# Kernel optimization log

Measured on AMD Instinct MI355X. Metric: run time of the kernel, lower is better.

The kernel has to match this reference:

```python
import jax, jax.numpy as jnp
import numpy as np

BETA = 0.25

def setup_inputs() -> dict:
    key = jax.random.key(0)
    k1, k2 = jax.random.split(key)
    N, D, K = 262144, 64, 512
    encoding = jax.random.normal(k1, (N, D), dtype=jnp.float32)
    # original inits uniform(-1/K, 1/K); scale a normal similarly is fine, but stay faithful:
    weight = jax.random.uniform(k2, (K, D), dtype=jnp.float32, minval=-1.0 / K, maxval=1.0 / K)
    return {"encoding": encoding, "weight": weight}


def reference(encoding, weight):
    # flat view: encoding already [N, D]
    x = encoding  # [N, D]
    # squared euclidean distances; argmin is invariant to sqrt and to ||x||^2 term
    x2 = jnp.sum(x * x, axis=1, keepdims=True)            # [N, 1]
    w2 = jnp.sum(weight * weight, axis=1)                  # [K]
    d2 = x2 - 2.0 * (x @ weight.T) + w2[None, :]           # [N, K]
    idx = jnp.argmin(d2, axis=1)                           # [N]
    quantized = weight[idx]                                # gather == one_hot @ weight, [N, D]

    commitment_loss = jnp.mean((jax.lax.stop_gradient(quantized) - x) ** 2)
    embedding_loss = jnp.mean((quantized - jax.lax.stop_gradient(x)) ** 2)
    vq_loss = commitment_loss * BETA + embedding_loss

    # straight-through estimator
    quantized_st = x + jax.lax.stop_gradient(quantized - x)
    return (idx[:, None], quantized_st, vq_loss)
```

## Files before the change

### kernel.cpp

```cpp
#include <hip/hip_runtime.h>

#define NROWS 262144
#define DDIM  64
#define KCB   512

#define MARGKEY (3u << 17)

#define WS_CNT   0
#define WS_W2P3  1024
#define WS_WHI   4096
#define WS_WMID  69632
#define WS_LIST  135168

typedef __attribute__((ext_vector_type(8))) short short8;
typedef __attribute__((ext_vector_type(4))) float floatx4;

__device__ __forceinline__ unsigned umin2(unsigned a, unsigned b) { return a < b ? a : b; }
__device__ __forceinline__ unsigned umax2(unsigned a, unsigned b) { return a > b ? a : b; }

__device__ __forceinline__ float np_sumsq64(const float* a) {
    float r[8];
#pragma unroll
    for (int j = 0; j < 8; ++j) r[j] = __fmul_rn(a[j], a[j]);
#pragma unroll
    for (int i = 8; i < 64; i += 8) {
#pragma unroll
        for (int j = 0; j < 8; ++j)
            r[j] = __fadd_rn(r[j], __fmul_rn(a[i + j], a[i + j]));
    }
    return __fadd_rn(__fadd_rn(__fadd_rn(r[0], r[1]), __fadd_rn(r[2], r[3])),
                     __fadd_rn(__fadd_rn(r[4], r[5]), __fadd_rn(r[6], r[7])));
}

__device__ __forceinline__ void split2(float e0, float e1, unsigned& hid, unsigned& mid) {
    unsigned u0 = __float_as_uint(e0), u1 = __float_as_uint(e1);
    float r0 = __fsub_rn(e0, __uint_as_float(u0 & 0xFFFF0000u));
    float r1 = __fsub_rn(e1, __uint_as_float(u1 & 0xFFFF0000u));
    hid = (u0 >> 16) | (u1 & 0xFFFF0000u);
    mid = (__float_as_uint(r0) >> 16) | (__float_as_uint(r1) & 0xFFFF0000u);
}

__global__ void vq_prep(const float* __restrict__ w, float* __restrict__ w2p3,
                        unsigned short* __restrict__ whi,
                        unsigned short* __restrict__ wmid) {
    const int k = threadIdx.x;
    float ws[64];
    const float4* wp = (const float4*)(w + (size_t)k * DDIM);
#pragma unroll
    for (int j = 0; j < 16; ++j) {
        float4 v = wp[j];
        ws[4 * j + 0] = v.x; ws[4 * j + 1] = v.y;
        ws[4 * j + 2] = v.z; ws[4 * j + 3] = v.w;
    }
    w2p3[k] = __fadd_rn(np_sumsq64(ws), 3.0f);
#pragma unroll
    for (int d = 0; d < 64; ++d) {
        float v = __fmul_rn(-2.0f, ws[d]);
        unsigned u = __float_as_uint(v);
        whi[k * 64 + d] = (unsigned short)(u >> 16);
        float rem = __fsub_rn(v, __uint_as_float(u & 0xFFFF0000u));
        wmid[k * 64 + d] = (unsigned short)(__float_as_uint(rem) >> 16);
    }
}

__launch_bounds__(512, 4)
__global__ void vq_gemm(const float* __restrict__ x,
                        const unsigned short* __restrict__ whi,
                        const unsigned short* __restrict__ wmid,
                        const float* __restrict__ w2p3g,
                        float* __restrict__ out_idx,
                        unsigned* __restrict__ cnt,
                        unsigned* __restrict__ list, int listcap) {
    const int tid = threadIdx.x;
    const int wave = tid >> 6, lane = tid & 63;
    const int n16 = lane & 15, quad = lane >> 4;

    __shared__ float w2p3s[KCB];
    __shared__ __align__(16) unsigned sbh[2][16 * 36];
    __shared__ __align__(16) unsigned sbm[2][16 * 36];
    __shared__ uint2 mm[8][32][16];

    w2p3s[tid] = w2p3g[tid];

    short8 ah[4][2], am[4][2];
#pragma unroll
    for (int f = 0; f < 4; ++f) {
        const int cw = wave * 64 + f * 16 + n16;
#pragma unroll
        for (int s = 0; s < 2; ++s) {
            ah[f][s] = *(const short8*)(whi + (size_t)cw * 64 + s * 32 + quad * 8);
            am[f][s] = *(const short8*)(wmid + (size_t)cw * 64 + s * 32 + quad * 8);
        }
    }

    const int r0 = blockIdx.x * 512;
    const int srow = tid >> 5, sj2 = tid & 31;
    {
        float2 v = *(const float2*)(x + (size_t)(r0 + srow) * DDIM + 2 * sj2);
        unsigned hid, mid; split2(v.x, v.y, hid, mid);
        sbh[0][srow * 36 + sj2] = hid;
        sbm[0][srow * 36 + sj2] = mid;
    }
    __syncthreads();

    const unsigned cwq = (unsigned)(wave * 64 + quad * 4);

    for (int it = 0; it < 32; ++it) {
        const int p = it & 1;
        float2 pre;
        if (it < 31)
            pre = *(const float2*)(x + (size_t)(r0 + (it + 1) * 16 + srow) * DDIM + 2 * sj2);

        short8 b_h0 = *(const short8*)&sbh[p][n16 * 36 + quad * 4];
        short8 b_h1 = *(const short8*)&sbh[p][n16 * 36 + 16 + quad * 4];
        short8 b_m0 = *(const short8*)&sbm[p][n16 * 36 + quad * 4];
        short8 b_m1 = *(const short8*)&sbm[p][n16 * 36 + 16 + quad * 4];

        floatx4 acc[4];
#pragma unroll
        for (int f = 0; f < 4; ++f)
            acc[f] = *(const floatx4*)&w2p3s[wave * 64 + f * 16 + quad * 4];
#pragma unroll
        for (int f = 0; f < 4; ++f) {
            acc[f] = __builtin_amdgcn_mfma_f32_16x16x32_bf16(ah[f][0], b_h0, acc[f], 0, 0, 0);
            acc[f] = __builtin_amdgcn_mfma_f32_16x16x32_bf16(ah[f][0], b_m0, acc[f], 0, 0, 0);
            acc[f] = __builtin_amdgcn_mfma_f32_16x16x32_bf16(am[f][0], b_h0, acc[f], 0, 0, 0);
            acc[f] = __builtin_amdgcn_mfma_f32_16x16x32_bf16(ah[f][1], b_h1, acc[f], 0, 0, 0);
            acc[f] = __builtin_amdgcn_mfma_f32_16x16x32_bf16(ah[f][1], b_m1, acc[f], 0, 0, 0);
            acc[f] = __builtin_amdgcn_mfma_f32_16x16x32_bf16(am[f][1], b_h1, acc[f], 0, 0, 0);
        }

        unsigned m1 = 0xFFFFFFFFu, m2 = 0xFFFFFFFFu;
#pragma unroll
        for (int f = 0; f < 4; ++f) {
#pragma unroll
            for (int reg = 0; reg < 4; ++reg) {
                unsigned key = (__float_as_uint(acc[f][reg]) << 9) +
                               (cwq + (unsigned)(f * 16 + reg));
                unsigned t = umax2(m1, key);
                m2 = umin2(m2, t);
                m1 = umin2(m1, key);
            }
        }
#pragma unroll
        for (int s = 16; s <= 32; s <<= 1) {
            unsigned o1 = __shfl_xor((int)m1, s);
            unsigned o2 = __shfl_xor((int)m2, s);
            m2 = umin2(umin2(m2, o2), umax2(m1, o1));
            m1 = umin2(m1, o1);
        }
        if (lane < 16) mm[wave][it][n16] = make_uint2(m1, m2);

        if (it < 31) {
            unsigned hid, mid; split2(pre.x, pre.y, hid, mid);
            sbh[p ^ 1][srow * 36 + sj2] = hid;
            sbm[p ^ 1][srow * 36 + sj2] = mid;
        }
        __syncthreads();
    }

    unsigned a1 = 0xFFFFFFFFu, a2 = 0xFFFFFFFFu;
#pragma unroll
    for (int wv = 0; wv < 8; ++wv) {
        uint2 v = mm[wv][tid >> 4][tid & 15];
        a2 = umin2(umin2(a2, v.y), umax2(a1, v.x));
        a1 = umin2(a1, v.x);
    }
    out_idx[r0 + tid] = (float)(a1 & 511u);
    bool flag = (a2 - a1 < MARGKEY);
    unsigned long long mask = __ballot(flag);
    int nw = __popcll(mask);
    unsigned base = 0;
    if (lane == 0 && nw) base = atomicAdd(cnt, (unsigned)nw);
    base = (unsigned)__shfl((int)base, 0);
    if (flag) {
        unsigned pos = base + (unsigned)__popcll(mask & ((1ull << lane) - 1ull));
        if ((int)pos < listcap) list[pos] = (unsigned)(r0 + tid);
    }
}

__launch_bounds__(512, 4)
__global__ void vq_recheck(const float* __restrict__ x,
                           const float* __restrict__ w,
                           const unsigned* __restrict__ cnt,
                           const unsigned* __restrict__ list, int listcap,
                           float* __restrict__ out_idx) {
    const int tid = threadIdx.x;
    unsigned total = *cnt;
    if (total > (unsigned)listcap) total = (unsigned)listcap;
    const unsigned nb = (total + 15) >> 4;

    float wl[64];
    {
        const float4* wp = (const float4*)(w + (size_t)tid * DDIM);
#pragma unroll
        for (int j = 0; j < 16; ++j) {
            float4 v = wp[j];
            wl[4 * j + 0] = v.x; wl[4 * j + 1] = v.y;
            wl[4 * j + 2] = v.z; wl[4 * j + 3] = v.w;
        }
    }
    const float w2l = np_sumsq64(wl);

    __shared__ float d2tile[16][KCB];
    __shared__ int rowbuf[16];
    __shared__ float x2buf[16];

    for (unsigned batch = blockIdx.x; batch < nb; batch += gridDim.x) {
        if (tid < 16) {
            unsigned li = batch * 16 + (unsigned)tid;
            rowbuf[tid] = (li < total) ? (int)list[li] : -1;
        }
        __syncthreads();

        if (tid < 128) {
            const int rl = tid >> 3, j = tid & 7;
            int row = rowbuf[rl]; if (row < 0) row = 0;
            const float* xr = x + (size_t)row * DDIM;
            float a0 = xr[j];
            float r = __fmul_rn(a0, a0);
#pragma unroll
            for (int i = 1; i < 8; ++i) {
                float ai = xr[8 * i + j];
                r = __fadd_rn(r, __fmul_rn(ai, ai));
            }
            float s1 = __fadd_rn(r,  __shfl_xor(r, 1));
            float s2 = __fadd_rn(s1, __shfl_xor(s1, 2));
            float s4 = __fadd_rn(s2, __shfl_xor(s2, 4));
            if (j == 0) x2buf[rl] = s4;
        }
        __syncthreads();

        for (int g = 0; g < 16; g += 4) {
            int ra = rowbuf[g + 0]; if (ra < 0) ra = 0;
            int rb = rowbuf[g + 1]; if (rb < 0) rb = 0;
            int rc = rowbuf[g + 2]; if (rc < 0) rc = 0;
            int rd = rowbuf[g + 3]; if (rd < 0) rd = 0;
            const float* xr0 = x + (size_t)ra * DDIM;
            const float* xr1 = x + (size_t)rb * DDIM;
            const float* xr2 = x + (size_t)rc * DDIM;
            const float* xr3 = x + (size_t)rd * DDIM;
            float m0 = 0.f, m1 = 0.f, m2 = 0.f, m3 = 0.f;
#pragma unroll
            for (int jb = 0; jb < 16; ++jb) {
                float4 a0 = *(const float4*)(xr0 + 4 * jb);
                float4 a1 = *(const float4*)(xr1 + 4 * jb);
                float4 a2 = *(const float4*)(xr2 + 4 * jb);
                float4 a3 = *(const float4*)(xr3 + 4 * jb);
                m0 = __fmaf_rn(a0.x, wl[4 * jb + 0], m0);
                m0 = __fmaf_rn(a0.y, wl[4 * jb + 1], m0);
                m0 = __fmaf_rn(a0.z, wl[4 * jb + 2], m0);
                m0 = __fmaf_rn(a0.w, wl[4 * jb + 3], m0);
                m1 = __fmaf_rn(a1.x, wl[4 * jb + 0], m1);
                m1 = __fmaf_rn(a1.y, wl[4 * jb + 1], m1);
                m1 = __fmaf_rn(a1.z, wl[4 * jb + 2], m1);
                m1 = __fmaf_rn(a1.w, wl[4 * jb + 3], m1);
                m2 = __fmaf_rn(a2.x, wl[4 * jb + 0], m2);
                m2 = __fmaf_rn(a2.y, wl[4 * jb + 1], m2);
                m2 = __fmaf_rn(a2.z, wl[4 * jb + 2], m2);
                m2 = __fmaf_rn(a2.w, wl[4 * jb + 3], m2);
                m3 = __fmaf_rn(a3.x, wl[4 * jb + 0], m3);
                m3 = __fmaf_rn(a3.y, wl[4 * jb + 1], m3);
                m3 = __fmaf_rn(a3.z, wl[4 * jb + 2], m3);
                m3 = __fmaf_rn(a3.w, wl[4 * jb + 3], m3);
            }
            float X0 = x2buf[g + 0], X1 = x2buf[g + 1];
            float X2 = x2buf[g + 2], X3 = x2buf[g + 3];
            d2tile[g + 0][tid] = __fadd_rn(__fsub_rn(X0, __fmul_rn(2.0f, m0)), w2l);
            d2tile[g + 1][tid] = __fadd_rn(__fsub_rn(X1, __fmul_rn(2.0f, m1)), w2l);
            d2tile[g + 2][tid] = __fadd_rn(__fsub_rn(X2, __fmul_rn(2.0f, m2)), w2l);
            d2tile[g + 3][tid] = __fadd_rn(__fsub_rn(X3, __fmul_rn(2.0f, m3)), w2l);
        }
        __syncthreads();

        {
            const int rl  = tid >> 5;
            const int sub = tid & 31;
            float bv = d2tile[rl][sub];
            int   bi = sub;
#pragma unroll
            for (int i = 1; i < 16; ++i) {
                int cc = sub + 32 * i;
                float v = d2tile[rl][cc];
                if (v < bv) { bv = v; bi = cc; }
            }
#pragma unroll
            for (int s = 1; s < 32; s <<= 1) {
                float ov = __shfl_xor(bv, s);
                int   oi = __shfl_xor(bi, s);
                if (ov < bv || (ov == bv && oi < bi)) { bv = ov; bi = oi; }
            }
            if (sub == 0 && rowbuf[rl] >= 0) out_idx[rowbuf[rl]] = (float)bi;
        }
        __syncthreads();
    }
}

__launch_bounds__(256)
__global__ void vq_epilogue(const float* __restrict__ x,
                            const float* __restrict__ w,
                            const float* __restrict__ out_idx_f,
                            float* __restrict__ out_q,
                            float* __restrict__ out_loss) {
    const int row  = blockIdx.x * blockDim.x + threadIdx.x;
    const int bidx = (int)out_idx_f[row];

    const float4* xp = (const float4*)(x + (size_t)row * DDIM);
    const float4* wq = (const float4*)(w + (size_t)bidx * DDIM);
    float4* qo = (float4*)(out_q + (size_t)row * DDIM);
    float ls = 0.0f;
#pragma unroll
    for (int j = 0; j < 16; ++j) {
        float4 xv = xp[j];
        float4 wv = wq[j];
        float e0 = __fsub_rn(wv.x, xv.x), e1 = __fsub_rn(wv.y, xv.y);
        float e2 = __fsub_rn(wv.z, xv.z), e3 = __fsub_rn(wv.w, xv.w);
        ls = fmaf(e0, e0, ls); ls = fmaf(e1, e1, ls);
        ls = fmaf(e2, e2, ls); ls = fmaf(e3, e3, ls);
        float4 q;
        q.x = __fadd_rn(xv.x, e0); q.y = __fadd_rn(xv.y, e1);
        q.z = __fadd_rn(xv.z, e2); q.w = __fadd_rn(xv.w, e3);
        qo[j] = q;
    }
#pragma unroll
    for (int off = 32; off > 0; off >>= 1) ls += __shfl_down(ls, off);
    __shared__ float red[4];
    const int lane = threadIdx.x & 63;
    const int wid  = threadIdx.x >> 6;
    if (lane == 0) red[wid] = ls;
    __syncthreads();
    if (threadIdx.x == 0) {
        float t = (red[0] + red[1]) + (red[2] + red[3]);
        atomicAdd(out_loss, t * (1.25f / (float)(NROWS * DDIM)));
    }
}

extern "C" void kernel_launch(void* const* d_in, const int* in_sizes, int n_in,
                              void* d_out, int out_size, void* d_ws, size_t ws_size,
                              hipStream_t stream) {
    const float* x = (const float*)d_in[0];
    const float* w = (const float*)d_in[1];

    float* out      = (float*)d_out;
    float* out_idx  = out;
    float* out_q    = out + (size_t)NROWS;
    float* out_loss = out + (size_t)NROWS + (size_t)NROWS * DDIM;

    char* ws = (char*)d_ws;
    unsigned* cnt  = (unsigned*)(ws + WS_CNT);
    float* w2p3    = (float*)(ws + WS_W2P3);
    unsigned short* whi  = (unsigned short*)(ws + WS_WHI);
    unsigned short* wmid = (unsigned short*)(ws + WS_WMID);
    unsigned* list = (unsigned*)(ws + WS_LIST);
    long cap = ((long)ws_size - WS_LIST) / 4;
    int listcap = cap > 0 ? (cap > NROWS ? NROWS : (int)cap) : 0;

    hipMemsetAsync(out_loss, 0, sizeof(float), stream);
    hipMemsetAsync(cnt, 0, sizeof(unsigned), stream);

    vq_prep<<<1, 512, 0, stream>>>(w, w2p3, whi, wmid);
    vq_gemm<<<NROWS / 512, 512, 0, stream>>>(x, whi, wmid, w2p3, out_idx, cnt, list, listcap);
    vq_recheck<<<256, 512, 0, stream>>>(x, w, cnt, list, listcap, out_idx);
    vq_epilogue<<<NROWS / 256, 256, 0, stream>>>(x, w, out_idx, out_q, out_loss);
}
```

Baseline: 253.2 us.

## Process 32 rows per iteration, widen loads, tree top-2, permlane swaps

```diff
diff --git a/kernel.cpp b/kernel.cpp
--- a/kernel.cpp
+++ b/kernel.cpp
@@ -14,6 +14,14 @@
 
 typedef __attribute__((ext_vector_type(8))) short short8;
 typedef __attribute__((ext_vector_type(4))) float floatx4;
+typedef __attribute__((ext_vector_type(2))) unsigned int uintx2;
+
+#if defined(__has_builtin)
+#if __has_builtin(__builtin_amdgcn_permlane16_swap) && \
+    __has_builtin(__builtin_amdgcn_permlane32_swap)
+#define VQ_PLSWAP 1
+#endif
+#endif
 
 __device__ __forceinline__ unsigned umin2(unsigned a, unsigned b) { return a < b ? a : b; }
 __device__ __forceinline__ unsigned umax2(unsigned a, unsigned b) { return a > b ? a : b; }
@@ -38,6 +46,42 @@
     float r1 = __fsub_rn(e1, __uint_as_float(u1 & 0xFFFF0000u));
     hid = (u0 >> 16) | (u1 & 0xFFFF0000u);
     mid = (__float_as_uint(r0) >> 16) | (__float_as_uint(r1) & 0xFFFF0000u);
+}
+
+__device__ __forceinline__ void split4(float4 v, uint2& h, uint2& m) {
+    unsigned h0, m0, h1, m1;
+    split2(v.x, v.y, h0, m0);
+    split2(v.z, v.w, h1, m1);
+    h = make_uint2(h0, h1);
+    m = make_uint2(m0, m1);
+}
+
+__device__ __forceinline__ void merge16(unsigned& m1, unsigned& m2) {
+#ifdef VQ_PLSWAP
+    uintx2 s1 = __builtin_amdgcn_permlane16_swap(m1, m1, false, false);
+    uintx2 s2 = __builtin_amdgcn_permlane16_swap(m2, m2, false, false);
+    m2 = umin2(umin2(s2[0], s2[1]), umax2(s1[0], s1[1]));
+    m1 = umin2(s1[0], s1[1]);
+#else
+    unsigned o1 = __shfl_xor((int)m1, 16);
+    unsigned o2 = __shfl_xor((int)m2, 16);
+    m2 = umin2(umin2(m2, o2), umax2(m1, o1));
+    m1 = umin2(m1, o1);
+#endif
+}
+
+__device__ __forceinline__ void merge32(unsigned& m1, unsigned& m2) {
+#ifdef VQ_PLSWAP
+    uintx2 s1 = __builtin_amdgcn_permlane32_swap(m1, m1, false, false);
+    uintx2 s2 = __builtin_amdgcn_permlane32_swap(m2, m2, false, false);
+    m2 = umin2(umin2(s2[0], s2[1]), umax2(s1[0], s1[1]));
+    m1 = umin2(s1[0], s1[1]);
+#else
+    unsigned o1 = __shfl_xor((int)m1, 32);
+    unsigned o2 = __shfl_xor((int)m2, 32);
+    m2 = umin2(umin2(m2, o2), umax2(m1, o1));
+    m1 = umin2(m1, o1);
+#endif
 }
 
 __global__ void vq_prep(const float* __restrict__ w, float* __restrict__ w2p3,
@@ -76,9 +120,9 @@
     const int n16 = lane & 15, quad = lane >> 4;
 
     __shared__ float w2p3s[KCB];
-    __shared__ __align__(16) unsigned sbh[2][16 * 36];
-    __shared__ __align__(16) unsigned sbm[2][16 * 36];
-    __shared__ uint2 mm[8][32][16];
+    __shared__ __align__(16) unsigned sbh[2][32 * 36];
+    __shared__ __align__(16) unsigned sbm[2][32 * 36];
+    __shared__ uint2 mm[8][16][32];
 
     w2p3s[tid] = w2p3g[tid];
 
@@ -94,67 +138,73 @@
     }
 
     const int r0 = blockIdx.x * 512;
-    const int srow = tid >> 5, sj2 = tid & 31;
+    const int srow = tid >> 4, sc4 = tid & 15;
     {
-        float2 v = *(const float2*)(x + (size_t)(r0 + srow) * DDIM + 2 * sj2);
-        unsigned hid, mid; split2(v.x, v.y, hid, mid);
-        sbh[0][srow * 36 + sj2] = hid;
-        sbm[0][srow * 36 + sj2] = mid;
+        float4 v = *(const float4*)(x + (size_t)(r0 + srow) * DDIM + 4 * sc4);
+        uint2 h, m; split4(v, h, m);
+        *(uint2*)&sbh[0][srow * 36 + 2 * sc4] = h;
+        *(uint2*)&sbm[0][srow * 36 + 2 * sc4] = m;
     }
     __syncthreads();
 
     const unsigned cwq = (unsigned)(wave * 64 + quad * 4);
 
-    for (int it = 0; it < 32; ++it) {
+    for (int it = 0; it < 16; ++it) {
         const int p = it & 1;
-        float2 pre;
-        if (it < 31)
-            pre = *(const float2*)(x + (size_t)(r0 + (it + 1) * 16 + srow) * DDIM + 2 * sj2);
-
-        short8 b_h0 = *(const short8*)&sbh[p][n16 * 36 + quad * 4];
-        short8 b_h1 = *(const short8*)&sbh[p][n16 * 36 + 16 + quad * 4];
-        short8 b_m0 = *(const short8*)&sbm[p][n16 * 36 + quad * 4];
-        short8 b_m1 = *(const short8*)&sbm[p][n16 * 36 + 16 + quad * 4];
-
-        floatx4 acc[4];
-#pragma unroll
-        for (int f = 0; f < 4; ++f)
-            acc[f] = *(const floatx4*)&w2p3s[wave * 64 + f * 16 + quad * 4];
-#pragma unroll
-        for (int f = 0; f < 4; ++f) {
-            acc[f] = __builtin_amdgcn_mfma_f32_16x16x32_bf16(ah[f][0], b_h0, acc[f], 0, 0, 0);
-            acc[f] = __builtin_amdgcn_mfma_f32_16x16x32_bf16(ah[f][0], b_m0, acc[f], 0, 0, 0);
-            acc[f] = __builtin_amdgcn_mfma_f32_16x16x32_bf16(am[f][0], b_h0, acc[f], 0, 0, 0);
-            acc[f] = __builtin_amdgcn_mfma_f32_16x16x32_bf16(ah[f][1], b_h1, acc[f], 0, 0, 0);
-            acc[f] = __builtin_amdgcn_mfma_f32_16x16x32_bf16(ah[f][1], b_m1, acc[f], 0, 0, 0);
-            acc[f] = __builtin_amdgcn_mfma_f32_16x16x32_bf16(am[f][1], b_h1, acc[f], 0, 0, 0);
-        }
-
-        unsigned m1 = 0xFFFFFFFFu, m2 = 0xFFFFFFFFu;
-#pragma unroll
-        for (int f = 0; f < 4; ++f) {
-#pragma unroll
-            for (int reg = 0; reg < 4; ++reg) {
-                unsigned key = (__float_as_uint(acc[f][reg]) << 9) +
-                               (cwq + (unsigned)(f * 16 + reg));
-                unsigned t = umax2(m1, key);
-                m2 = umin2(m2, t);
-                m1 = umin2(m1, key);
-            }
-        }
-#pragma unroll
-        for (int s = 16; s <= 32; s <<= 1) {
-            unsigned o1 = __shfl_xor((int)m1, s);
-            unsigned o2 = __shfl_xor((int)m2, s);
-            m2 = umin2(umin2(m2, o2), umax2(m1, o1));
-            m1 = umin2(m1, o1);
-        }
-        if (lane < 16) mm[wave][it][n16] = make_uint2(m1, m2);
-
-        if (it < 31) {
-            unsigned hid, mid; split2(pre.x, pre.y, hid, mid);
-            sbh[p ^ 1][srow * 36 + sj2] = hid;
-            sbm[p ^ 1][srow * 36 + sj2] = mid;
+        float4 pre;
+        if (it < 15)
+            pre = *(const float4*)(x + (size_t)(r0 + (it + 1) * 32 + srow) * DDIM + 4 * sc4);
+
+#pragma unroll
+        for (int sub = 0; sub < 2; ++sub) {
+            const int rb = (sub * 16 + n16) * 36;
+            short8 b_h0 = *(const short8*)&sbh[p][rb + quad * 4];
+            short8 b_h1 = *(const short8*)&sbh[p][rb + 16 + quad * 4];
+            short8 b_m0 = *(const short8*)&sbm[p][rb + quad * 4];
+            short8 b_m1 = *(const short8*)&sbm[p][rb + 16 + quad * 4];
+
+            floatx4 acc[4];
+#pragma unroll
+            for (int f = 0; f < 4; ++f)
+                acc[f] = *(const floatx4*)&w2p3s[wave * 64 + f * 16 + quad * 4];
+#pragma unroll
+            for (int f = 0; f < 4; ++f) {
+                acc[f] = __builtin_amdgcn_mfma_f32_16x16x32_bf16(ah[f][0], b_h0, acc[f], 0, 0, 0);
+                acc[f] = __builtin_amdgcn_mfma_f32_16x16x32_bf16(ah[f][0], b_m0, acc[f], 0, 0, 0);
+                acc[f] = __builtin_amdgcn_mfma_f32_16x16x32_bf16(am[f][0], b_h0, acc[f], 0, 0, 0);
+                acc[f] = __builtin_amdgcn_mfma_f32_16x16x32_bf16(ah[f][1], b_h1, acc[f], 0, 0, 0);
+                acc[f] = __builtin_amdgcn_mfma_f32_16x16x32_bf16(ah[f][1], b_m1, acc[f], 0, 0, 0);
+                acc[f] = __builtin_amdgcn_mfma_f32_16x16x32_bf16(am[f][1], b_h1, acc[f], 0, 0, 0);
+            }
+
+            unsigned p1[4], p2[4];
+#pragma unroll
+            for (int f = 0; f < 4; ++f) {
+                unsigned k0 = (__float_as_uint(acc[f][0]) << 9) + (cwq + (unsigned)(f * 16 + 0));
+                unsigned k1 = (__float_as_uint(acc[f][1]) << 9) + (cwq + (unsigned)(f * 16 + 1));
+                unsigned k2 = (__float_as_uint(acc[f][2]) << 9) + (cwq + (unsigned)(f * 16 + 2));
+                unsigned k3 = (__float_as_uint(acc[f][3]) << 9) + (cwq + (unsigned)(f * 16 + 3));
+                unsigned lo01 = umin2(k0, k1), hi01 = umax2(k0, k1);
+                unsigned lo23 = umin2(k2, k3), hi23 = umax2(k2, k3);
+                p1[f] = umin2(lo01, lo23);
+                p2[f] = umin2(umax2(lo01, lo23), umin2(hi01, hi23));
+            }
+            unsigned q1a = umin2(p1[0], p1[1]);
+            unsigned q2a = umin2(umax2(p1[0], p1[1]), umin2(p2[0], p2[1]));
+            unsigned q1b = umin2(p1[2], p1[3]);
+            unsigned q2b = umin2(umax2(p1[2], p1[3]), umin2(p2[2], p2[3]));
+            unsigned m1 = umin2(q1a, q1b);
+            unsigned m2 = umin2(umax2(q1a, q1b), umin2(q2a, q2b));
+
+            merge16(m1, m2);
+            merge32(m1, m2);
+            if (lane < 16) mm[wave][it][sub * 16 + n16] = make_uint2(m1, m2);
+        }
+
+        if (it < 15) {
+            uint2 h, m; split4(pre, h, m);
+            *(uint2*)&sbh[p ^ 1][srow * 36 + 2 * sc4] = h;
+            *(uint2*)&sbm[p ^ 1][srow * 36 + 2 * sc4] = m;
         }
         __syncthreads();
     }
@@ -162,7 +212,7 @@
     unsigned a1 = 0xFFFFFFFFu, a2 = 0xFFFFFFFFu;
 #pragma unroll
     for (int wv = 0; wv < 8; ++wv) {
-        uint2 v = mm[wv][tid >> 4][tid & 15];
+        uint2 v = mm[wv][tid >> 5][tid & 31];
         a2 = umin2(umin2(a2, v.y), umax2(a1, v.x));
         a1 = umin2(a1, v.x);
     }
@@ -189,6 +239,7 @@
     unsigned total = *cnt;
     if (total > (unsigned)listcap) total = (unsigned)listcap;
     const unsigned nb = (total + 15) >> 4;
+    if (blockIdx.x >= nb) return;
 
     float wl[64];
     {
```

After: 255.6 us. About the same (+1.0%).
